# Kernel optimization log

Hardware: AMD Instinct MI355X
Metric: run time of the kernel (lower is better)

Reference implementation:

```python
import jax, jax.numpy as jnp
import numpy as np


def setup_inputs() -> dict:
    key = jax.random.key(0)
    ks = jax.random.split(key, 8)
    b, l, d_model = 2, 2048, 1024
    d_inner, d_state, dt_rank, d_conv = 2048, 16, 64, 4
    g = lambda k, shape, s: jax.random.normal(k, shape, jnp.float32) * s
    A = jnp.broadcast_to(jnp.arange(1, d_state + 1, dtype=jnp.float32), (d_inner, d_state))
    return {
        "x": g(ks[0], (b, l, d_model), 1.0),
        "W_in": g(ks[1], (d_model, 2 * d_inner), 0.02),
        "W_conv": g(ks[2], (d_inner, 1, d_conv), 0.1),
        "b_conv": g(ks[3], (d_inner,), 0.1),
        "W_x": g(ks[4], (d_inner, dt_rank + 2 * d_state), 0.02),
        "W_dt": g(ks[5], (dt_rank, d_inner), 0.02),
        "b_dt": g(ks[6], (d_inner,), 0.1),
        "A_log": jnp.log(A),
        "D": jnp.ones((d_inner,), jnp.float32),
        "W_out": g(ks[7], (d_inner, d_model), 0.02),
    }


def _selective_scan(x, delta, A, B, C, D):
    # x, delta: (b, l, d); A: (d, n); B, C: (b, l, n); D: (d,)
    b, l, d = x.shape
    n = A.shape[1]

    def step(h, inp):
        dt, Bt, Ct, xt = inp  # (b,d), (b,n), (b,n), (b,d)
        dA = jnp.exp(dt[:, :, None] * A)                     # (b,d,n)
        h = dA * h + (dt * xt)[:, :, None] * Bt[:, None, :]  # (b,d,n)
        y = jnp.einsum('bdn,bn->bd', h, Ct)
        return h, y

    h0 = jnp.zeros((b, d, n), x.dtype)
    xs = (jnp.swapaxes(delta, 0, 1), jnp.swapaxes(B, 0, 1),
          jnp.swapaxes(C, 0, 1), jnp.swapaxes(x, 0, 1))
    _, ys = jax.lax.scan(step, h0, xs)   # ys: (l, b, d)
    return jnp.swapaxes(ys, 0, 1) + D * x


def _mamba(x, W_in, W_conv, b_conv, W_x, W_dt, b_dt, A_log, D, W_out):
    b, l, _ = x.shape
    d_inner = W_conv.shape[0]
    d_conv = W_conv.shape[2]
    dt_rank = W_dt.shape[0]
    n = A_log.shape[1]

    xr = x @ W_in                                   # (b,l,2*d_inner)
    xin, res = xr[..., :d_inner], xr[..., d_inner:]

    # depthwise causal conv1d (left pad d_conv-1 == torch pad both + trim to l)
    xc = jnp.swapaxes(xin, 1, 2)                    # (b,d_inner,l)
    xc = jax.lax.conv_general_dilated(
        xc, W_conv, window_strides=(1,), padding=[(d_conv - 1, 0)],
        feature_group_count=d_inner,
        dimension_numbers=('NCH', 'OIH', 'NCH')) + b_conv[None, :, None]
    xs = jax.nn.silu(jnp.swapaxes(xc, 1, 2))        # (b,l,d_inner)

    x_dbl = xs @ W_x                                # (b,l,dt_rank+2n)
    delta = jax.nn.softplus(x_dbl[..., :dt_rank] @ W_dt + b_dt)
    Bm = x_dbl[..., dt_rank:dt_rank + n]
    Cm = x_dbl[..., dt_rank + n:]
    A = -jnp.exp(A_log)

    y = _selective_scan(xs, delta, A, Bm, Cm, D)
    y = y * jax.nn.silu(res)
    return y @ W_out


def reference(x, W_in, W_conv, b_conv, W_x, W_dt, b_dt, A_log, D, W_out):
    return _mamba(x, W_in, W_conv, b_conv, W_x, W_dt, b_dt, A_log, D, W_out)
```

## Files before the change

kernel.cpp:

```cpp
#include <hip/hip_runtime.h>


typedef unsigned short ushort_t;
using short8 = __attribute__((ext_vector_type(8))) short;
using f32x4  = __attribute__((ext_vector_type(4))) float;
using gptr_t = const __attribute__((address_space(1))) unsigned short*;
using sptr_t = __attribute__((address_space(3))) unsigned short*;

#define NC 64
#define CL 32

__device__ inline ushort_t f2bf(float v) {
    unsigned u = __float_as_uint(v);
    unsigned r = (u + 0x7fff + ((u >> 16) & 1)) >> 16;
    return (ushort_t)r;
}
__device__ inline float bf2f(ushort_t h) { return __uint_as_float(((unsigned)h) << 16); }
__device__ inline void split2(float v, ushort_t& h, ushort_t& l) {
    h = f2bf(v);
    l = f2bf(v - bf2f(h));
}

__global__ __launch_bounds__(256) void convert_all(
    const float* __restrict__ x, ushort_t* __restrict__ xh, ushort_t* __restrict__ xl,
    const float* __restrict__ W_in, ushort_t* __restrict__ winh, ushort_t* __restrict__ winl,
    const float* __restrict__ W_out, ushort_t* __restrict__ wouth, ushort_t* __restrict__ woutl,
    const float* __restrict__ W_x, ushort_t* __restrict__ wxh, ushort_t* __restrict__ wxl,
    const float* __restrict__ W_dt, ushort_t* __restrict__ wdth, ushort_t* __restrict__ wdtl) {
    __shared__ float tile[32][33];
    const int id = blockIdx.x;
    if (id < 4096) {
        int i = id * 256 + threadIdx.x;
        float4 v = ((const float4*)x)[i];
        ushort4 hh, ll;
        split2(v.x, hh.x, ll.x); split2(v.y, hh.y, ll.y);
        split2(v.z, hh.z, ll.z); split2(v.w, hh.w, ll.w);
        ((ushort4*)xh)[i] = hh;
        ((ushort4*)xl)[i] = ll;
        return;
    }
    const float* W; ushort_t *Th, *Tl; int K, N, bx, by;
    if (id < 8192)       { W = W_in;  Th = winh;  Tl = winl;  K = 1024; N = 4096;
                           bx = (id - 4096) & 127; by = (id - 4096) >> 7; }
    else if (id < 10240) { W = W_out; Th = wouth; Tl = woutl; K = 2048; N = 1024;
                           bx = (id - 8192) & 31;  by = (id - 8192) >> 5; }
    else if (id < 10496) { W = W_x;   Th = wxh;   Tl = wxl;   K = 2048; N = 96;
                           bx = (id - 10240) & 3;  by = (id - 10240) >> 2; }
    else                 { W = W_dt;  Th = wdth;  Tl = wdtl;  K = 64;   N = 2048;
                           bx = (id - 10496) & 63; by = (id - 10496) >> 6; }
    int n0 = bx * 32, k0 = by * 32;
    int tx = threadIdx.x & 31, ty = threadIdx.x >> 5;
    #pragma unroll
    for (int j = 0; j < 4; ++j) {
        int k = ty + j * 8;
        tile[k][tx] = (n0 + tx < N) ? W[(size_t)(k0 + k) * N + n0 + tx] : 0.f;
    }
    __syncthreads();
    #pragma unroll
    for (int j = 0; j < 4; ++j) {
        int nrow = ty + j * 8;
        float v = tile[tx][nrow];
        ushort_t h, l;
        split2(v, h, l);
        size_t o = (size_t)(n0 + nrow) * K + k0 + tx;
        Th[o] = h; Tl[o] = l;
    }
}

__global__ __launch_bounds__(512, 2) void gemm_mfma3_256(
    const ushort_t* __restrict__ Ah, const ushort_t* __restrict__ Al,
    const ushort_t* __restrict__ Bh, const ushort_t* __restrict__ Bl,
    float* __restrict__ C, int M, int N, int K) {
    __shared__ ushort_t lds[65536];
    const int tid  = threadIdx.x;
    const int w    = tid >> 6;
    const int lane = tid & 63;
    const int wr = w >> 2;
    const int wc = w & 3;
    const int fr = lane & 15;
    const int kq = (lane >> 4) * 8;
    const int bm = blockIdx.y * 256;
    const int bn = blockIdx.x * 256;
    const int NT = K >> 5;

    const int sg   = tid ^ ((tid >> 3) & 7);
    const int srow = sg >> 2;
    const int skof = (sg & 3) * 8;

    f32x4 acc[8][4];
    #pragma unroll
    for (int i = 0; i < 8; ++i)
        #pragma unroll
        for (int j = 0; j < 4; ++j) acc[i][j] = (f32x4){0.f, 0.f, 0.f, 0.f};

    #define STAGE(t, db)                                                          \
    {                                                                             \
        const int k0_ = (t) * 32;                                                 \
        _Pragma("unroll")                                                         \
        for (int h_ = 0; h_ < 2; ++h_) {                                          \
            const size_t ga_ = (size_t)(bm + h_ * 128 + srow) * K + k0_ + skof;   \
            const size_t gb_ = (size_t)(bn + h_ * 128 + srow) * K + k0_ + skof;   \
            const int dst_ = (db) * 8192 + h_ * 4096 + w * 512;                   \
            __builtin_amdgcn_global_load_lds((gptr_t)(Ah + ga_), (sptr_t)&lds[0     + dst_], 16, 0, 0); \
            __builtin_amdgcn_global_load_lds((gptr_t)(Al + ga_), (sptr_t)&lds[16384 + dst_], 16, 0, 0); \
            __builtin_amdgcn_global_load_lds((gptr_t)(Bh + gb_), (sptr_t)&lds[32768 + dst_], 16, 0, 0); \
            __builtin_amdgcn_global_load_lds((gptr_t)(Bl + gb_), (sptr_t)&lds[49152 + dst_], 16, 0, 0); \
        }                                                                         \
    }

    #define LDF(arrOff, db, row) \
        (*(const short8*)&lds[(arrOff) + (db) * 8192 + \
            ((((row) << 2) | (kq >> 3)) ^ (((row) >> 1) & 7)) * 8])

    STAGE(0, 0);
    STAGE(1, 1);
    asm volatile("s_waitcnt vmcnt(8)" ::: "memory");
    __builtin_amdgcn_s_barrier();

    for (int t = 0; t < NT; ++t) {
        const int db = t & 1;
        short8 bhF[4], blF[4], ahF[4], alF[4];
        #pragma unroll
        for (int j = 0; j < 4; ++j) {
            const int row = 128 + wc * 32 + j * 16 + fr - 128;
            (void)row;
        }
        #pragma unroll
        for (int j = 0; j < 4; ++j) {
            const int rowb = wc * 64 + j * 16 + fr;
            bhF[j] = LDF(32768, db, rowb);
            blF[j] = LDF(49152, db, rowb);
        }
        #pragma unroll
        for (int i = 0; i < 4; ++i) {
            const int rowa = wr * 128 + i * 16 + fr;
            ahF[i] = LDF(0, db, rowa);
            alF[i] = LDF(16384, db, rowa);
        }
        __builtin_amdgcn_s_setprio(1);
        #pragma unroll
        for (int i = 0; i < 4; ++i)
            #pragma unroll
            for (int j = 0; j < 4; ++j) {
                acc[i][j] = __builtin_amdgcn_mfma_f32_16x16x32_bf16(ahF[i], bhF[j], acc[i][j], 0, 0, 0);
                acc[i][j] = __builtin_amdgcn_mfma_f32_16x16x32_bf16(ahF[i], blF[j], acc[i][j], 0, 0, 0);
                acc[i][j] = __builtin_amdgcn_mfma_f32_16x16x32_bf16(alF[i], bhF[j], acc[i][j], 0, 0, 0);
            }
        __builtin_amdgcn_s_setprio(0);
        short8 ah2[4], al2[4];
        #pragma unroll
        for (int i = 0; i < 4; ++i) {
            const int rowa = wr * 128 + (i + 4) * 16 + fr;
            ah2[i] = LDF(0, db, rowa);
            al2[i] = LDF(16384, db, rowa);
        }
        asm volatile("s_waitcnt lgkmcnt(0)" ::: "memory");
        __builtin_amdgcn_sched_barrier(0);
        __builtin_amdgcn_s_barrier();
        if (t + 2 < NT) STAGE(t + 2, db);
        __builtin_amdgcn_s_setprio(1);
        #pragma unroll
        for (int i = 0; i < 4; ++i)
            #pragma unroll
            for (int j = 0; j < 4; ++j) {
                acc[i + 4][j] = __builtin_amdgcn_mfma_f32_16x16x32_bf16(ah2[i], bhF[j], acc[i + 4][j], 0, 0, 0);
                acc[i + 4][j] = __builtin_amdgcn_mfma_f32_16x16x32_bf16(ah2[i], blF[j], acc[i + 4][j], 0, 0, 0);
                acc[i + 4][j] = __builtin_amdgcn_mfma_f32_16x16x32_bf16(al2[i], bhF[j], acc[i + 4][j], 0, 0, 0);
            }
        __builtin_amdgcn_s_setprio(0);
        if (t + 2 < NT) {
            asm volatile("s_waitcnt vmcnt(8)" ::: "memory");
        } else {
            asm volatile("s_waitcnt vmcnt(0)" ::: "memory");
        }
        __builtin_amdgcn_sched_barrier(0);
        __builtin_amdgcn_s_barrier();
    }
    #undef STAGE
    #undef LDF

    #pragma unroll
    for (int i = 0; i < 8; ++i) {
        const int row = bm + wr * 128 + i * 16 + (lane >> 4) * 4;
        #pragma unroll
        for (int j = 0; j < 4; ++j) {
            const int col = bn + wc * 64 + j * 16 + fr;
            float* cp = C + (size_t)row * N + col;
            #pragma unroll
            for (int r = 0; r < 4; ++r) cp[(size_t)r * N] = acc[i][j][r];
        }
    }
}

__global__ __launch_bounds__(256) void gemm_mfma3(
    const ushort_t* __restrict__ Ah, const ushort_t* __restrict__ Al,
    const ushort_t* __restrict__ Bh, const ushort_t* __restrict__ Bl,
    float* __restrict__ C, int M, int N, int K,
    const float* __restrict__ bias, int epi) {
    __shared__ ushort_t sAh[4096], sAl[4096], sBh[4096], sBl[4096];
    const int tid  = threadIdx.x;
    const int wid  = tid >> 6;
    const int lane = tid & 63;
    const int bm = blockIdx.y * 128;
    const int bn = blockIdx.x * 128;
    const int wr = wid >> 1, wc = wid & 1;

    f32x4 acc[4][4];
    #pragma unroll
    for (int i = 0; i < 4; ++i)
        #pragma unroll
        for (int j = 0; j < 4; ++j) acc[i][j] = (f32x4){0.f, 0.f, 0.f, 0.f};

    for (int k0 = 0; k0 < K; k0 += 32) {
        #pragma unroll
        for (int issue = 0; issue < 2; ++issue) {
            const int off = wid * 2048 + issue * 1024 + lane * 16;
            const int row = off >> 6;
            const int ce  = (off & 63) >> 1;
            const size_t ga = (size_t)(bm + row) * K + k0 + ce;
            const size_t gb = (size_t)(bn + row) * K + k0 + ce;
            const int lo = (wid * 2048 + issue * 1024) >> 1;
            __builtin_amdgcn_global_load_lds((gptr_t)(Ah + ga), (sptr_t)&sAh[lo], 16, 0, 0);
            __builtin_amdgcn_global_load_lds((gptr_t)(Al + ga), (sptr_t)&sAl[lo], 16, 0, 0);
            __builtin_amdgcn_global_load_lds((gptr_t)(Bh + gb), (sptr_t)&sBh[lo], 16, 0, 0);
            __builtin_amdgcn_global_load_lds((gptr_t)(Bl + gb), (sptr_t)&sBl[lo], 16, 0, 0);
        }
        __syncthreads();

        const int fr = lane & 15;
        const int kb = (lane >> 4) * 8;
        short8 ah[4], al[4], bh[4], bl[4];
        #pragma unroll
        for (int i = 0; i < 4; ++i) {
            const int ra = (wr * 64 + i * 16 + fr) * 32 + kb;
            ah[i] = *(const short8*)&sAh[ra];
            al[i] = *(const short8*)&sAl[ra];
            const int rb = (wc * 64 + i * 16 + fr) * 32 + kb;
            bh[i] = *(const short8*)&sBh[rb];
            bl[i] = *(const short8*)&sBl[rb];
        }
        #pragma unroll
        for (int i = 0; i < 4; ++i)
            #pragma unroll
            for (int j = 0; j < 4; ++j) {
                acc[i][j] = __builtin_amdgcn_mfma_f32_16x16x32_bf16(ah[i], bh[j], acc[i][j], 0, 0, 0);
                acc[i][j] = __builtin_amdgcn_mfma_f32_16x16x32_bf16(ah[i], bl[j], acc[i][j], 0, 0, 0);
                acc[i][j] = __builtin_amdgcn_mfma_f32_16x16x32_bf16(al[i], bh[j], acc[i][j], 0, 0, 0);
            }
        __syncthreads();
    }

    #pragma unroll
    for (int i = 0; i < 4; ++i) {
        int row = bm + wr * 64 + i * 16 + (lane >> 4) * 4;
        #pragma unroll
        for (int j = 0; j < 4; ++j) {
            int col = bn + wc * 64 + j * 16 + (lane & 15);
            float* cp = C + (size_t)row * N + col;
            #pragma unroll
            for (int r = 0; r < 4; ++r) {
                float v = acc[i][j][r];
                if (epi == 1) {
                    v += bias[col];
                    v = (v > 20.f) ? v : log1pf(__expf(v));
                }
                cp[(size_t)r * N] = v;
            }
        }
    }
}

__global__ __launch_bounds__(256) void gemm_mfma3_n64(
    const ushort_t* __restrict__ Ah, const ushort_t* __restrict__ Al,
    const ushort_t* __restrict__ Bh, const ushort_t* __restrict__ Bl,
    float* __restrict__ C, int M, int N, int K) {
    __shared__ ushort_t sAh[4096], sAl[4096], sBh[2048], sBl[2048];
    const int tid  = threadIdx.x;
    const int wid  = tid >> 6;
    const int lane = tid & 63;
    const int bm = blockIdx.y * 128;
    const int bn = blockIdx.x * 64;
    const int wr = wid >> 1, wc = wid & 1;

    f32x4 acc[4][2];
    #pragma unroll
    for (int i = 0; i < 4; ++i)
        #pragma unroll
        for (int j = 0; j < 2; ++j) acc[i][j] = (f32x4){0.f, 0.f, 0.f, 0.f};

    for (int k0 = 0; k0 < K; k0 += 32) {
        #pragma unroll
        for (int issue = 0; issue < 2; ++issue) {
            const int off = issue * 4096 + tid * 16;
            const int row = off >> 6;
            const int ce  = (off & 63) >> 1;
            const size_t ga = (size_t)(bm + row) * K + k0 + ce;
            const int lo = (issue * 4096 + wid * 1024) >> 1;
            __builtin_amdgcn_global_load_lds((gptr_t)(Ah + ga), (sptr_t)&sAh[lo], 16, 0, 0);
            __builtin_amdgcn_global_load_lds((gptr_t)(Al + ga), (sptr_t)&sAl[lo], 16, 0, 0);
        }
        {
            const int off = tid * 16;
            const int row = off >> 6;
            const int ce  = (off & 63) >> 1;
            const size_t gb = (size_t)(bn + row) * K + k0 + ce;
            const int lo = (wid * 1024) >> 1;
            __builtin_amdgcn_global_load_lds((gptr_t)(Bh + gb), (sptr_t)&sBh[lo], 16, 0, 0);
            __builtin_amdgcn_global_load_lds((gptr_t)(Bl + gb), (sptr_t)&sBl[lo], 16, 0, 0);
        }
        __syncthreads();

        const int fr = lane & 15;
        const int kb = (lane >> 4) * 8;
        short8 ah[4], al[4], bh[2], bl[2];
        #pragma unroll
        for (int i = 0; i < 4; ++i) {
            const int ra = (wr * 64 + i * 16 + fr) * 32 + kb;
            ah[i] = *(const short8*)&sAh[ra];
            al[i] = *(const short8*)&sAl[ra];
        }
        #pragma unroll
        for (int j = 0; j < 2; ++j) {
            const int rb = (wc * 32 + j * 16 + fr) * 32 + kb;
            bh[j] = *(const short8*)&sBh[rb];
            bl[j] = *(const short8*)&sBl[rb];
        }
        #pragma unroll
        for (int i = 0; i < 4; ++i)
            #pragma unroll
            for (int j = 0; j < 2; ++j) {
                acc[i][j] = __builtin_amdgcn_mfma_f32_16x16x32_bf16(ah[i], bh[j], acc[i][j], 0, 0, 0);
                acc[i][j] = __builtin_amdgcn_mfma_f32_16x16x32_bf16(ah[i], bl[j], acc[i][j], 0, 0, 0);
                acc[i][j] = __builtin_amdgcn_mfma_f32_16x16x32_bf16(al[i], bh[j], acc[i][j], 0, 0, 0);
            }
        __syncthreads();
    }

    #pragma unroll
    for (int i = 0; i < 4; ++i) {
        int row = bm + wr * 64 + i * 16 + (lane >> 4) * 4;
        #pragma unroll
        for (int j = 0; j < 2; ++j) {
            int col = bn + wc * 32 + j * 16 + (lane & 15);
            float* cp = C + (size_t)row * N + col;
            #pragma unroll
            for (int r = 0; r < 4; ++r) cp[(size_t)r * N] = acc[i][j][r];
        }
    }
}

__global__ __launch_bounds__(256) void gemm_mfma3_sk(
    const ushort_t* __restrict__ Ah, const ushort_t* __restrict__ Al,
    const ushort_t* __restrict__ Bh, const ushort_t* __restrict__ Bl,
    float* __restrict__ partial, int K) {
    __shared__ ushort_t sAh[4096], sAl[4096], sBh[4096], sBl[4096];
    const int tid  = threadIdx.x;
    const int wid  = tid >> 6;
    const int lane = tid & 63;
    const int kslice = blockIdx.x;
    const int bm = blockIdx.y * 128;
    const int wr = wid >> 1, wc = wid & 1;
    const int kbeg = kslice * 128;

    f32x4 acc[4][4];
    #pragma unroll
    for (int i = 0; i < 4; ++i)
        #pragma unroll
        for (int j = 0; j < 4; ++j) acc[i][j] = (f32x4){0.f, 0.f, 0.f, 0.f};

    for (int k0 = kbeg; k0 < kbeg + 128; k0 += 32) {
        #pragma unroll
        for (int issue = 0; issue < 2; ++issue) {
            const int off = wid * 2048 + issue * 1024 + lane * 16;
            const int row = off >> 6;
            const int ce  = (off & 63) >> 1;
            const size_t ga = (size_t)(bm + row) * K + k0 + ce;
            const size_t gb = (size_t)row * K + k0 + ce;
            const int lo = (wid * 2048 + issue * 1024) >> 1;
            __builtin_amdgcn_global_load_lds((gptr_t)(Ah + ga), (sptr_t)&sAh[lo], 16, 0, 0);
            __builtin_amdgcn_global_load_lds((gptr_t)(Al + ga), (sptr_t)&sAl[lo], 16, 0, 0);
            __builtin_amdgcn_global_load_lds((gptr_t)(Bh + gb), (sptr_t)&sBh[lo], 16, 0, 0);
            __builtin_amdgcn_global_load_lds((gptr_t)(Bl + gb), (sptr_t)&sBl[lo], 16, 0, 0);
        }
        __syncthreads();

        const int fr = lane & 15;
        const int kb = (lane >> 4) * 8;
        short8 ah[4], al[4], bh[4], bl[4];
        #pragma unroll
        for (int i = 0; i < 4; ++i) {
            const int ra = (wr * 64 + i * 16 + fr) * 32 + kb;
            ah[i] = *(const short8*)&sAh[ra];
            al[i] = *(const short8*)&sAl[ra];
            const int rb = (wc * 64 + i * 16 + fr) * 32 + kb;
            bh[i] = *(const short8*)&sBh[rb];
            bl[i] = *(const short8*)&sBl[rb];
        }
        #pragma unroll
        for (int i = 0; i < 4; ++i)
            #pragma unroll
            for (int j = 0; j < 4; ++j) {
                acc[i][j] = __builtin_amdgcn_mfma_f32_16x16x32_bf16(ah[i], bh[j], acc[i][j], 0, 0, 0);
                acc[i][j] = __builtin_amdgcn_mfma_f32_16x16x32_bf16(ah[i], bl[j], acc[i][j], 0, 0, 0);
                acc[i][j] = __builtin_amdgcn_mfma_f32_16x16x32_bf16(al[i], bh[j], acc[i][j], 0, 0, 0);
            }
        __syncthreads();
    }

    float* Cp = partial + (size_t)kslice * 4096 * 96;
    #pragma unroll
    for (int i = 0; i < 4; ++i) {
        int row = bm + wr * 64 + i * 16 + (lane >> 4) * 4;
        #pragma unroll
        for (int j = 0; j < 4; ++j) {
            int col = wc * 64 + j * 16 + (lane & 15);
            if (col < 96) {
                float* cp = Cp + (size_t)row * 96 + col;
                #pragma unroll
                for (int r = 0; r < 4; ++r) cp[(size_t)r * 96] = acc[i][j][r];
            }
        }
    }
}

__global__ void reduce16split(const float4* __restrict__ p, float4* __restrict__ xdbl4,
                              ushort_t* __restrict__ dh, ushort_t* __restrict__ dl) {
    int i = blockIdx.x * 256 + threadIdx.x;
    float4 s = p[i];
    #pragma unroll
    for (int k = 1; k < 16; ++k) {
        float4 v = p[i + k * 98304];
        s.x += v.x; s.y += v.y; s.z += v.z; s.w += v.w;
    }
    int row = i / 24;
    int c4  = i - row * 24;
    xdbl4[row * 32 + c4] = s;
    if (c4 < 16) {
        ushort4 hh, ll;
        split2(s.x, hh.x, ll.x); split2(s.y, hh.y, ll.y);
        split2(s.z, hh.z, ll.z); split2(s.w, hh.w, ll.w);
        ((ushort4*)dh)[row * 16 + c4] = hh;
        ((ushort4*)dl)[row * 16 + c4] = ll;
    }
}

__global__ void conv_silu_k(const float* __restrict__ xr, const float* __restrict__ Wc,
                            const float* __restrict__ bc,
                            ushort_t* __restrict__ xsh, ushort_t* __restrict__ xsl,
                            int total) {
    for (int idx = blockIdx.x * blockDim.x + threadIdx.x; idx < total;
         idx += gridDim.x * blockDim.x) {
        int d = idx & 2047;
        int l = (idx >> 11) & 2047;
        int b = idx >> 22;
        float acc = bc[d];
        const float* wp = Wc + d * 4;
        #pragma unroll
        for (int k = 0; k < 4; ++k) {
            int ll = l - 3 + k;
            if (ll >= 0)
                acc = fmaf(xr[((size_t)(b * 2048 + ll) << 12) + d], wp[k], acc);
        }
        float v = acc / (1.f + __expf(-acc));
        ushort_t h, lo;
        split2(v, h, lo);
        xsh[idx] = h;
        xsl[idx] = lo;
    }
}

__global__ __launch_bounds__(256) void scan_p1(
    const float* __restrict__ delta,
    const ushort_t* __restrict__ xsh, const ushort_t* __restrict__ xsl,
    const float* __restrict__ xdbl, const float* __restrict__ A_log,
    float* __restrict__ S, float* __restrict__ sumdt) {
    const int u = blockIdx.x * 256 + threadIdx.x;
    const int chunk = u >> 12;
    const int c = u & 4095;
    const int b = c >> 11, d = c & 2047;

    float a[16];
    #pragma unroll
    for (int i = 0; i < 4; ++i) {
        float4 v = ((const float4*)(A_log + d * 16))[i];
        a[4 * i + 0] = -__expf(v.x); a[4 * i + 1] = -__expf(v.y);
        a[4 * i + 2] = -__expf(v.z); a[4 * i + 3] = -__expf(v.w);
    }
    float h[16];
    #pragma unroll
    for (int n = 0; n < 16; ++n) h[n] = 0.f;
    float sdt = 0.f;

    const size_t row0 = (size_t)b * 2048 + (size_t)chunk * CL;
    const float4* xd4 = (const float4*)xdbl;
    #pragma unroll 2
    for (int t = 0; t < CL; ++t) {
        const size_t row = row0 + t;
        float dt = delta[row * 2048 + d];
        float xv = bf2f(xsh[row * 2048 + d]) + bf2f(xsl[row * 2048 + d]);
        float4 Bv[4];
        #pragma unroll
        for (int i = 0; i < 4; ++i) Bv[i] = xd4[row * 32 + 16 + i];
        const float* Bf = (const float*)Bv;
        sdt += dt;
        float du = dt * xv;
        #pragma unroll
        for (int n = 0; n < 16; ++n) {
            float dA = __expf(dt * a[n]);
            h[n] = fmaf(dA, h[n], du * Bf[n]);
        }
    }
    float4* S4 = (float4*)(S + ((size_t)chunk * 4096 + c) * 16);
    #pragma unroll
    for (int i = 0; i < 4; ++i)
        S4[i] = make_float4(h[4 * i + 0], h[4 * i + 1], h[4 * i + 2], h[4 * i + 3]);
    sumdt[chunk * 4096 + c] = sdt;
}

__global__ __launch_bounds__(256) void scan_p2(
    float* __restrict__ S, const float* __restrict__ sumdt,
    const float* __restrict__ A_log) {
    const int idx = blockIdx.x * blockDim.x + threadIdx.x;
    const int n = idx & 15;
    const int c = (idx >> 4) & 4095;
    const int d = c & 2047;
    const float a = -__expf(A_log[d * 16 + n]);
    float h = 0.f;
    for (int k = 0; k < NC; ++k) {
        const size_t o = ((size_t)k * 4096 + c) * 16 + n;
        float carry = S[o];
        S[o] = h;
        float P = __expf(a * sumdt[k * 4096 + c]);
        h = fmaf(P, h, carry);
    }
}

__global__ __launch_bounds__(256) void scan_p3(
    const float* __restrict__ delta,
    const ushort_t* __restrict__ xsh, const ushort_t* __restrict__ xsl,
    const float* __restrict__ xdbl, const float* __restrict__ xr,
    const float* __restrict__ A_log, const float* __restrict__ Dp,
    const float* __restrict__ H0,
    ushort_t* __restrict__ yh, ushort_t* __restrict__ yl) {
    const int u = blockIdx.x * 256 + threadIdx.x;
    const int chunk = u >> 12;
    const int c = u & 4095;
    const int b = c >> 11, d = c & 2047;

    float a[16];
    #pragma unroll
    for (int i = 0; i < 4; ++i) {
        float4 v = ((const float4*)(A_log + d * 16))[i];
        a[4 * i + 0] = -__expf(v.x); a[4 * i + 1] = -__expf(v.y);
        a[4 * i + 2] = -__expf(v.z); a[4 * i + 3] = -__expf(v.w);
    }
    float h[16];
    const float4* H4 = (const float4*)(H0 + ((size_t)chunk * 4096 + c) * 16);
    #pragma unroll
    for (int i = 0; i < 4; ++i) {
        float4 v = H4[i];
        h[4 * i + 0] = v.x; h[4 * i + 1] = v.y; h[4 * i + 2] = v.z; h[4 * i + 3] = v.w;
    }
    const float Dd = Dp[d];

    const size_t row0 = (size_t)b * 2048 + (size_t)chunk * CL;
    const float4* xd4 = (const float4*)xdbl;
    #pragma unroll 2
    for (int t = 0; t < CL; ++t) {
        const size_t row = row0 + t;
        float dt = delta[row * 2048 + d];
        float xv = bf2f(xsh[row * 2048 + d]) + bf2f(xsl[row * 2048 + d]);
        float4 BC[8];
        #pragma unroll
        for (int i = 0; i < 8; ++i) BC[i] = xd4[row * 32 + 16 + i];
        const float* Bf = (const float*)BC;
        const float* Cf = Bf + 16;
        float du = dt * xv;
        float acc = 0.f;
        #pragma unroll
        for (int n = 0; n < 16; ++n) {
            float dA = __expf(dt * a[n]);
            h[n] = fmaf(dA, h[n], du * Bf[n]);
            acc = fmaf(h[n], Cf[n], acc);
        }
        float rv = xr[(row << 12) + 2048 + d];
        float yv = fmaf(Dd, xv, acc) * (rv / (1.f + __expf(-rv)));
        ushort_t hb, lb;
        split2(yv, hb, lb);
        yh[row * 2048 + d] = hb;
        yl[row * 2048 + d] = lb;
    }
}

extern "C" void kernel_launch(void* const* d_in, const int* in_sizes, int n_in,
                              void* d_out, int out_size, void* d_ws, size_t ws_size,
                              hipStream_t stream) {
    const float* x      = (const float*)d_in[0];
    const float* W_in   = (const float*)d_in[1];
    const float* W_conv = (const float*)d_in[2];
    const float* b_conv = (const float*)d_in[3];
    const float* W_x    = (const float*)d_in[4];
    const float* W_dt   = (const float*)d_in[5];
    const float* b_dt   = (const float*)d_in[6];
    const float* A_log  = (const float*)d_in[7];
    const float* Dp     = (const float*)d_in[8];
    const float* W_out  = (const float*)d_in[9];
    float* out = (float*)d_out;

    float* ws    = (float*)d_ws;
    float* xr    = ws;
    float* xdbl  = xr + 16777216;
    float* delta = xdbl + 524288;
    float* S     = delta + 8388608;
    float* sumdt = S + 4194304;
    ushort_t* base = (ushort_t*)(sumdt + 262144);
    ushort_t* xh = base, *xl = base + 4194304;
    ushort_t* winh = base + 8388608, *winl = base + 12582912;
    float*    partial = (float*)base;
    ushort_t* yh = base, *yl = base + 8388608;
    ushort_t* wouth = base + 16777216, *woutl = base + 18874368;
    ushort_t* wxh   = base + 20971520, *wxl   = base + 21233664;
    ushort_t* wdth  = base + 21495808, *wdtl  = base + 21626880;
    ushort_t* dAh   = base + 21757952, *dAl   = base + 22020096;
    ushort_t* xsh   = base + 22282240, *xsl   = base + 30670848;

    dim3 blk(256);

    convert_all<<<dim3(10624), blk, 0, stream>>>(x, xh, xl, W_in, winh, winl,
                                                 W_out, wouth, woutl,
                                                 W_x, wxh, wxl, W_dt, wdth, wdtl);

    gemm_mfma3_256<<<dim3(16, 16), dim3(512), 0, stream>>>(xh, xl, winh, winl, xr,
                                                           4096, 4096, 1024);
    conv_silu_k<<<dim3(4096), blk, 0, stream>>>(xr, W_conv, b_conv, xsh, xsl, 8388608);
    gemm_mfma3_sk<<<dim3(16, 32), blk, 0, stream>>>(xsh, xsl, wxh, wxl, partial, 2048);
    reduce16split<<<dim3(384), blk, 0, stream>>>((const float4*)partial, (float4*)xdbl,
                                                 dAh, dAl);
    gemm_mfma3<<<dim3(16, 32), blk, 0, stream>>>(dAh, dAl, wdth, wdtl, delta,
                                                 4096, 2048, 64, b_dt, 1);
    scan_p1<<<dim3(1024), blk, 0, stream>>>(delta, xsh, xsl, xdbl, A_log, S, sumdt);
    scan_p2<<<dim3(256), blk, 0, stream>>>(S, sumdt, A_log);
    scan_p3<<<dim3(1024), blk, 0, stream>>>(delta, xsh, xsl, xdbl, xr, A_log, Dp, S, yh, yl);
    gemm_mfma3_n64<<<dim3(16, 32), blk, 0, stream>>>(yh, yl, wouth, woutl, out,
                                                     4096, 1024, 2048);
}
```

Before: 509.3 us.

## Fuse delta projection into split-K reduce; split-K 256-tile GEMM for output

The dt projection GEMM (K=64) and its bf16 split conversion are replaced with an fp32 FMA computation inside the split-K reduction kernel, which also applies bias and softplus. This removes one GEMM launch, the dA high/low conversion buffers and the W_dt conversion. The output projection now reuses the large 256x256 tile GEMM with a 4-way split-K over a z grid dimension, followed by a separate reduce4 kernel. That adds partial-buffer traffic in exchange for better occupancy and tile reuse. The delta path is now computed in fp32 rather than three bf16 MFMA products.

```diff
diff --git a/kernel.cpp b/kernel.cpp
--- a/kernel.cpp
+++ b/kernel.cpp
@@ -25,8 +25,7 @@
     const float* __restrict__ x, ushort_t* __restrict__ xh, ushort_t* __restrict__ xl,
     const float* __restrict__ W_in, ushort_t* __restrict__ winh, ushort_t* __restrict__ winl,
     const float* __restrict__ W_out, ushort_t* __restrict__ wouth, ushort_t* __restrict__ woutl,
-    const float* __restrict__ W_x, ushort_t* __restrict__ wxh, ushort_t* __restrict__ wxl,
-    const float* __restrict__ W_dt, ushort_t* __restrict__ wdth, ushort_t* __restrict__ wdtl) {
+    const float* __restrict__ W_x, ushort_t* __restrict__ wxh, ushort_t* __restrict__ wxl) {
     __shared__ float tile[32][33];
     const int id = blockIdx.x;
     if (id < 4096) {
@@ -44,10 +43,8 @@
                            bx = (id - 4096) & 127; by = (id - 4096) >> 7; }
     else if (id < 10240) { W = W_out; Th = wouth; Tl = woutl; K = 2048; N = 1024;
                            bx = (id - 8192) & 31;  by = (id - 8192) >> 5; }
-    else if (id < 10496) { W = W_x;   Th = wxh;   Tl = wxl;   K = 2048; N = 96;
+    else                 { W = W_x;   Th = wxh;   Tl = wxl;   K = 2048; N = 96;
                            bx = (id - 10240) & 3;  by = (id - 10240) >> 2; }
-    else                 { W = W_dt;  Th = wdth;  Tl = wdtl;  K = 64;   N = 2048;
-                           bx = (id - 10496) & 63; by = (id - 10496) >> 6; }
     int n0 = bx * 32, k0 = by * 32;
     int tx = threadIdx.x & 31, ty = threadIdx.x >> 5;
     #pragma unroll
@@ -70,7 +67,7 @@
 __global__ __launch_bounds__(512, 2) void gemm_mfma3_256(
     const ushort_t* __restrict__ Ah, const ushort_t* __restrict__ Al,
     const ushort_t* __restrict__ Bh, const ushort_t* __restrict__ Bl,
-    float* __restrict__ C, int M, int N, int K) {
+    float* __restrict__ C, int M, int N, int K, int ksteps, int partial_stride) {
     __shared__ ushort_t lds[65536];
     const int tid  = threadIdx.x;
     const int w    = tid >> 6;
@@ -81,7 +78,9 @@
     const int kq = (lane >> 4) * 8;
     const int bm = blockIdx.y * 256;
     const int bn = blockIdx.x * 256;
-    const int NT = K >> 5;
+    const int NT = ksteps;
+    const int kbeg = blockIdx.z * ksteps * 32;
+    C += (size_t)blockIdx.z * partial_stride;
 
     const int sg   = tid ^ ((tid >> 3) & 7);
     const int srow = sg >> 2;
@@ -95,7 +94,7 @@
 
     #define STAGE(t, db)                                                          \
     {                                                                             \
-        const int k0_ = (t) * 32;                                                 \
+        const int k0_ = kbeg + (t) * 32;                                          \
         _Pragma("unroll")                                                         \
         for (int h_ = 0; h_ < 2; ++h_) {                                          \
             const size_t ga_ = (size_t)(bm + h_ * 128 + srow) * K + k0_ + skof;   \
@@ -120,11 +119,6 @@
     for (int t = 0; t < NT; ++t) {
         const int db = t & 1;
         short8 bhF[4], blF[4], ahF[4], alF[4];
-        #pragma unroll
-        for (int j = 0; j < 4; ++j) {
-            const int row = 128 + wc * 32 + j * 16 + fr - 128;
-            (void)row;
-        }
         #pragma unroll
         for (int j = 0; j < 4; ++j) {
             const int rowb = wc * 64 + j * 16 + fr;
@@ -192,161 +186,15 @@
     }
 }
 
-__global__ __launch_bounds__(256) void gemm_mfma3(
-    const ushort_t* __restrict__ Ah, const ushort_t* __restrict__ Al,
-    const ushort_t* __restrict__ Bh, const ushort_t* __restrict__ Bl,
-    float* __restrict__ C, int M, int N, int K,
-    const float* __restrict__ bias, int epi) {
-    __shared__ ushort_t sAh[4096], sAl[4096], sBh[4096], sBl[4096];
-    const int tid  = threadIdx.x;
-    const int wid  = tid >> 6;
-    const int lane = tid & 63;
-    const int bm = blockIdx.y * 128;
-    const int bn = blockIdx.x * 128;
-    const int wr = wid >> 1, wc = wid & 1;
-
-    f32x4 acc[4][4];
-    #pragma unroll
-    for (int i = 0; i < 4; ++i)
-        #pragma unroll
-        for (int j = 0; j < 4; ++j) acc[i][j] = (f32x4){0.f, 0.f, 0.f, 0.f};
-
-    for (int k0 = 0; k0 < K; k0 += 32) {
-        #pragma unroll
-        for (int issue = 0; issue < 2; ++issue) {
-            const int off = wid * 2048 + issue * 1024 + lane * 16;
-            const int row = off >> 6;
-            const int ce  = (off & 63) >> 1;
-            const size_t ga = (size_t)(bm + row) * K + k0 + ce;
-            const size_t gb = (size_t)(bn + row) * K + k0 + ce;
-            const int lo = (wid * 2048 + issue * 1024) >> 1;
-            __builtin_amdgcn_global_load_lds((gptr_t)(Ah + ga), (sptr_t)&sAh[lo], 16, 0, 0);
-            __builtin_amdgcn_global_load_lds((gptr_t)(Al + ga), (sptr_t)&sAl[lo], 16, 0, 0);
-            __builtin_amdgcn_global_load_lds((gptr_t)(Bh + gb), (sptr_t)&sBh[lo], 16, 0, 0);
-            __builtin_amdgcn_global_load_lds((gptr_t)(Bl + gb), (sptr_t)&sBl[lo], 16, 0, 0);
-        }
-        __syncthreads();
-
-        const int fr = lane & 15;
-        const int kb = (lane >> 4) * 8;
-        short8 ah[4], al[4], bh[4], bl[4];
-        #pragma unroll
-        for (int i = 0; i < 4; ++i) {
-            const int ra = (wr * 64 + i * 16 + fr) * 32 + kb;
-            ah[i] = *(const short8*)&sAh[ra];
-            al[i] = *(const short8*)&sAl[ra];
-            const int rb = (wc * 64 + i * 16 + fr) * 32 + kb;
-            bh[i] = *(const short8*)&sBh[rb];
-            bl[i] = *(const short8*)&sBl[rb];
-        }
-        #pragma unroll
-        for (int i = 0; i < 4; ++i)
-            #pragma unroll
-            for (int j = 0; j < 4; ++j) {
-                acc[i][j] = __builtin_amdgcn_mfma_f32_16x16x32_bf16(ah[i], bh[j], acc[i][j], 0, 0, 0);
-                acc[i][j] = __builtin_amdgcn_mfma_f32_16x16x32_bf16(ah[i], bl[j], acc[i][j], 0, 0, 0);
-                acc[i][j] = __builtin_amdgcn_mfma_f32_16x16x32_bf16(al[i], bh[j], acc[i][j], 0, 0, 0);
-            }
-        __syncthreads();
-    }
-
-    #pragma unroll
-    for (int i = 0; i < 4; ++i) {
-        int row = bm + wr * 64 + i * 16 + (lane >> 4) * 4;
-        #pragma unroll
-        for (int j = 0; j < 4; ++j) {
-            int col = bn + wc * 64 + j * 16 + (lane & 15);
-            float* cp = C + (size_t)row * N + col;
-            #pragma unroll
-            for (int r = 0; r < 4; ++r) {
-                float v = acc[i][j][r];
-                if (epi == 1) {
-                    v += bias[col];
-                    v = (v > 20.f) ? v : log1pf(__expf(v));
-                }
-                cp[(size_t)r * N] = v;
-            }
-        }
-    }
-}
-
-__global__ __launch_bounds__(256) void gemm_mfma3_n64(
-    const ushort_t* __restrict__ Ah, const ushort_t* __restrict__ Al,
-    const ushort_t* __restrict__ Bh, const ushort_t* __restrict__ Bl,
-    float* __restrict__ C, int M, int N, int K) {
-    __shared__ ushort_t sAh[4096], sAl[4096], sBh[2048], sBl[2048];
-    const int tid  = threadIdx.x;
-    const int wid  = tid >> 6;
-    const int lane = tid & 63;
-    const int bm = blockIdx.y * 128;
-    const int bn = blockIdx.x * 64;
-    const int wr = wid >> 1, wc = wid & 1;
-
-    f32x4 acc[4][2];
-    #pragma unroll
-    for (int i = 0; i < 4; ++i)
-        #pragma unroll
-        for (int j = 0; j < 2; ++j) acc[i][j] = (f32x4){0.f, 0.f, 0.f, 0.f};
-
-    for (int k0 = 0; k0 < K; k0 += 32) {
-        #pragma unroll
-        for (int issue = 0; issue < 2; ++issue) {
-            const int off = issue * 4096 + tid * 16;
-            const int row = off >> 6;
-            const int ce  = (off & 63) >> 1;
-            const size_t ga = (size_t)(bm + row) * K + k0 + ce;
-            const int lo = (issue * 4096 + wid * 1024) >> 1;
-            __builtin_amdgcn_global_load_lds((gptr_t)(Ah + ga), (sptr_t)&sAh[lo], 16, 0, 0);
-            __builtin_amdgcn_global_load_lds((gptr_t)(Al + ga), (sptr_t)&sAl[lo], 16, 0, 0);
-        }
-        {
-            const int off = tid * 16;
-            const int row = off >> 6;
-            const int ce  = (off & 63) >> 1;
-            const size_t gb = (size_t)(bn + row) * K + k0 + ce;
-            const int lo = (wid * 1024) >> 1;
-            __builtin_amdgcn_global_load_lds((gptr_t)(Bh + gb), (sptr_t)&sBh[lo], 16, 0, 0);
-            __builtin_amdgcn_global_load_lds((gptr_t)(Bl + gb), (sptr_t)&sBl[lo], 16, 0, 0);
-        }
-        __syncthreads();
-
-        const int fr = lane & 15;
-        const int kb = (lane >> 4) * 8;
-        short8 ah[4], al[4], bh[2], bl[2];
-        #pragma unroll
-        for (int i = 0; i < 4; ++i) {
-            const int ra = (wr * 64 + i * 16 + fr) * 32 + kb;
-            ah[i] = *(const short8*)&sAh[ra];
-            al[i] = *(const short8*)&sAl[ra];
-        }
-        #pragma unroll
-        for (int j = 0; j < 2; ++j) {
-            const int rb = (wc * 32 + j * 16 + fr) * 32 + kb;
-            bh[j] = *(const short8*)&sBh[rb];
-            bl[j] = *(const short8*)&sBl[rb];
-        }
-        #pragma unroll
-        for (int i = 0; i < 4; ++i)
-            #pragma unroll
-            for (int j = 0; j < 2; ++j) {
-                acc[i][j] = __builtin_amdgcn_mfma_f32_16x16x32_bf16(ah[i], bh[j], acc[i][j], 0, 0, 0);
-                acc[i][j] = __builtin_amdgcn_mfma_f32_16x16x32_bf16(ah[i], bl[j], acc[i][j], 0, 0, 0);
-                acc[i][j] = __builtin_amdgcn_mfma_f32_16x16x32_bf16(al[i], bh[j], acc[i][j], 0, 0, 0);
-            }
-        __syncthreads();
-    }
-
-    #pragma unroll
-    for (int i = 0; i < 4; ++i) {
-        int row = bm + wr * 64 + i * 16 + (lane >> 4) * 4;
-        #pragma unroll
-        for (int j = 0; j < 2; ++j) {
-            int col = bn + wc * 32 + j * 16 + (lane & 15);
-            float* cp = C + (size_t)row * N + col;
-            #pragma unroll
-            for (int r = 0; r < 4; ++r) cp[(size_t)r * N] = acc[i][j][r];
-        }
-    }
+__global__ void reduce4(const float4* __restrict__ p, float4* __restrict__ outp) {
+    int i = blockIdx.x * 256 + threadIdx.x;
+    float4 s = p[i];
+    #pragma unroll
+    for (int k = 1; k < 4; ++k) {
+        float4 v = p[i + (size_t)k * 1048576];
+        s.x += v.x; s.y += v.y; s.z += v.z; s.w += v.w;
+    }
+    outp[i] = s;
 }
 
 __global__ __launch_bounds__(256) void gemm_mfma3_sk(
@@ -423,24 +271,59 @@
     }
 }
 
-__global__ void reduce16split(const float4* __restrict__ p, float4* __restrict__ xdbl4,
-                              ushort_t* __restrict__ dh, ushort_t* __restrict__ dl) {
-    int i = blockIdx.x * 256 + threadIdx.x;
-    float4 s = p[i];
-    #pragma unroll
-    for (int k = 1; k < 16; ++k) {
-        float4 v = p[i + k * 98304];
-        s.x += v.x; s.y += v.y; s.z += v.z; s.w += v.w;
-    }
-    int row = i / 24;
-    int c4  = i - row * 24;
-    xdbl4[row * 32 + c4] = s;
-    if (c4 < 16) {
-        ushort4 hh, ll;
-        split2(s.x, hh.x, ll.x); split2(s.y, hh.y, ll.y);
-        split2(s.z, hh.z, ll.z); split2(s.w, hh.w, ll.w);
-        ((ushort4*)dh)[row * 16 + c4] = hh;
-        ((ushort4*)dl)[row * 16 + c4] = ll;
+__global__ __launch_bounds__(256) void reduce_delta(
+    const float4* __restrict__ p,
+    float* __restrict__ xdbl,
+    const float* __restrict__ W_dt,
+    const float* __restrict__ b_dt,
+    float* __restrict__ delta) {
+    __shared__ float rows[16][96];
+    const int r0 = blockIdx.x * 16;
+    for (int j = threadIdx.x; j < 384; j += 256) {
+        int row = j / 24, c4 = j % 24;
+        size_t idx = (size_t)(r0 + row) * 24 + c4;
+        float4 s = p[idx];
+        #pragma unroll
+        for (int k = 1; k < 16; ++k) {
+            float4 v = p[idx + (size_t)k * 98304];
+            s.x += v.x; s.y += v.y; s.z += v.z; s.w += v.w;
+        }
+        *(float4*)&rows[row][c4 * 4] = s;
+        if (c4 >= 16)
+            ((float4*)(xdbl + (size_t)(r0 + row) * 128))[c4] = s;
+    }
+    __syncthreads();
+    const int c = threadIdx.x * 8;
+    float acc[16][8];
+    #pragma unroll
+    for (int r = 0; r < 16; ++r)
+        #pragma unroll
+        for (int j = 0; j < 8; ++j) acc[r][j] = 0.f;
+    for (int k = 0; k < 64; ++k) {
+        float4 w0 = *(const float4*)&W_dt[(size_t)k * 2048 + c];
+        float4 w1 = *(const float4*)&W_dt[(size_t)k * 2048 + c + 4];
+        float wv[8] = {w0.x, w0.y, w0.z, w0.w, w1.x, w1.y, w1.z, w1.w};
+        #pragma unroll
+        for (int r = 0; r < 16; ++r) {
+            float dv = rows[r][k];
+            #pragma unroll
+            for (int j = 0; j < 8; ++j) acc[r][j] = fmaf(dv, wv[j], acc[r][j]);
+        }
+    }
+    float4 b0 = *(const float4*)&b_dt[c];
+    float4 b1 = *(const float4*)&b_dt[c + 4];
+    float bv[8] = {b0.x, b0.y, b0.z, b0.w, b1.x, b1.y, b1.z, b1.w};
+    #pragma unroll
+    for (int r = 0; r < 16; ++r) {
+        float o[8];
+        #pragma unroll
+        for (int j = 0; j < 8; ++j) {
+            float v = acc[r][j] + bv[j];
+            o[j] = (v > 20.f) ? v : log1pf(__expf(v));
+        }
+        float* dp = delta + (size_t)(r0 + r) * 2048 + c;
+        *(float4*)dp       = make_float4(o[0], o[1], o[2], o[3]);
+        *(float4*)(dp + 4) = make_float4(o[4], o[5], o[6], o[7]);
     }
 }
 
@@ -620,27 +503,24 @@
     ushort_t* yh = base, *yl = base + 8388608;
     ushort_t* wouth = base + 16777216, *woutl = base + 18874368;
     ushort_t* wxh   = base + 20971520, *wxl   = base + 21233664;
-    ushort_t* wdth  = base + 21495808, *wdtl  = base + 21626880;
-    ushort_t* dAh   = base + 21757952, *dAl   = base + 22020096;
     ushort_t* xsh   = base + 22282240, *xsl   = base + 30670848;
+    float* outPartial = xr;
 
     dim3 blk(256);
 
-    convert_all<<<dim3(10624), blk, 0, stream>>>(x, xh, xl, W_in, winh, winl,
-                                                 W_out, wouth, woutl,
-                                                 W_x, wxh, wxl, W_dt, wdth, wdtl);
-
-    gemm_mfma3_256<<<dim3(16, 16), dim3(512), 0, stream>>>(xh, xl, winh, winl, xr,
-                                                           4096, 4096, 1024);
+    convert_all<<<dim3(10496), blk, 0, stream>>>(x, xh, xl, W_in, winh, winl,
+                                                 W_out, wouth, woutl, W_x, wxh, wxl);
+
+    gemm_mfma3_256<<<dim3(16, 16, 1), dim3(512), 0, stream>>>(
+        xh, xl, winh, winl, xr, 4096, 4096, 1024, 32, 0);
     conv_silu_k<<<dim3(4096), blk, 0, stream>>>(xr, W_conv, b_conv, xsh, xsl, 8388608);
     gemm_mfma3_sk<<<dim3(16, 32), blk, 0, stream>>>(xsh, xsl, wxh, wxl, partial, 2048);
-    reduce16split<<<dim3(384), blk, 0, stream>>>((const float4*)partial, (float4*)xdbl,
-                                                 dAh, dAl);
-    gemm_mfma3<<<dim3(16, 32), blk, 0, stream>>>(dAh, dAl, wdth, wdtl, delta,
-                                                 4096, 2048, 64, b_dt, 1);
+    reduce_delta<<<dim3(256), blk, 0, stream>>>((const float4*)partial, xdbl,
+                                                W_dt, b_dt, delta);
     scan_p1<<<dim3(1024), blk, 0, stream>>>(delta, xsh, xsl, xdbl, A_log, S, sumdt);
     scan_p2<<<dim3(256), blk, 0, stream>>>(S, sumdt, A_log);
     scan_p3<<<dim3(1024), blk, 0, stream>>>(delta, xsh, xsl, xdbl, xr, A_log, Dp, S, yh, yl);
-    gemm_mfma3_n64<<<dim3(16, 32), blk, 0, stream>>>(yh, yl, wouth, woutl, out,
-                                                     4096, 1024, 2048);
-}
+    gemm_mfma3_256<<<dim3(4, 16, 4), dim3(512), 0, stream>>>(
+        yh, yl, wouth, woutl, outPartial, 4096, 1024, 2048, 16, 4194304);
+    reduce4<<<dim3(4096), blk, 0, stream>>>((const float4*)outPartial, (float4*)out);
+}
```

New measurement: 544.2 us. +6.9%, slower.
